# Kernel optimization log

Hardware: AMD Instinct MI355X
Metric: run time of the kernel (lower is better)

Reference implementation:

```python
import jax, jax.numpy as jnp
import numpy as np

B, P, D, H, A, C = 256, 512, 16, 256, 8, 2
HID = 256
IN_MLP = H + A + 1  # 265


def setup_inputs() -> dict:
    key = jax.random.key(0)
    ks = jax.random.split(key, 12)
    s = 0.05  # small init for recurrent stability
    return {
        "particles": jax.random.normal(ks[0], (B, P, D), jnp.float32),
        "weights": jax.random.uniform(ks[1], (B, P), jnp.float32),
        "actions": jax.random.normal(ks[2], (B, A), jnp.float32),
        "time": jax.random.uniform(ks[3], (B,), jnp.float32) * 100.0,
        "Wi": jax.random.normal(ks[4], (D + 1, 3 * H), jnp.float32) * s,
        "bi": jnp.zeros((3 * H,), jnp.float32),
        "Wh_rz": jax.random.normal(ks[5], (H, 2 * H), jnp.float32) * s,
        "Wh_n": jax.random.normal(ks[6], (H, H), jnp.float32) * s,
        "bn": jnp.zeros((H,), jnp.float32),
        "mlp_W1": jax.random.normal(ks[7], (C, IN_MLP, HID), jnp.float32) * s,
        "mlp_b1": jnp.zeros((C, HID), jnp.float32),
        "mlp_W2": jax.random.normal(ks[8], (C, HID, HID), jnp.float32) * s,
        "mlp_b2": jnp.zeros((C, HID), jnp.float32),
        "mlp_W3": jax.random.normal(ks[9], (C, HID, 1), jnp.float32) * s,
        "mlp_b3": jnp.zeros((C, 1), jnp.float32),
        "num_time_steps": 100,
    }


def reference(particles, weights, actions, time, Wi, bi, Wh_rz, Wh_n, bn,
              mlp_W1, mlp_b1, mlp_W2, mlp_b2, mlp_W3, mlp_b3, num_time_steps):
    # feature_fn = identity; append weights as an extra feature channel
    x = jnp.concatenate([particles, weights[..., None]], axis=-1)  # [B, P, D+1]
    xs = jnp.swapaxes(x, 0, 1)  # [P, B, D+1], scan over particle axis

    def gru_step(h, xt):
        gi = xt @ Wi + bi  # [B, 3H]
        i_r, i_z, i_n = jnp.split(gi, 3, axis=-1)
        hrz = h @ Wh_rz  # [B, 2H], no bias (flax GRUCell hidden r/z dense)
        r = jax.nn.sigmoid(i_r + hrz[:, :H])
        z = jax.nn.sigmoid(i_z + hrz[:, H:])
        n = jnp.tanh(i_n + r * (h @ Wh_n + bn))
        h_new = (1.0 - z) * n + z * h
        return h_new, None

    h0 = jnp.zeros((particles.shape[0], H), particles.dtype)
    enc, _ = jax.lax.scan(gru_step, h0, xs)  # last hidden == take(outputs, -1, axis=-2)

    norm_time = time / num_time_steps
    hidden = jnp.concatenate([enc, actions, norm_time[..., None]], axis=-1)  # [B, IN_MLP]

    # n_critics MLPs evaluated batched over critic axis c
    h1 = jax.nn.relu(jnp.einsum('bi,cio->bco', hidden, mlp_W1) + mlp_b1)
    h2 = jax.nn.relu(jnp.einsum('bci,cio->bco', h1, mlp_W2) + mlp_b2)
    q = jnp.einsum('bci,cio->bco', h2, mlp_W3) + mlp_b3  # [B, C, 1]
    return q[..., 0]  # [B, C]
```

## Files before the change

kernel.cpp:

```cpp
#include <hip/hip_runtime.h>
#include <hip/hip_fp16.h>

typedef _Float16 h2v __attribute__((ext_vector_type(2)));
typedef _Float16 f16x8 __attribute__((ext_vector_type(8)));
typedef float f32x4 __attribute__((ext_vector_type(4)));
typedef unsigned int u32;
typedef unsigned short u16;

#define NB 256
#define NP 512
#define NH 256

#define OFF_WH 0
#define LEN_WH 98304
#define OFF_WIB (OFF_WH + LEN_WH)
#define LEN_WIB 12288
#define OFF_W1 (OFF_WIB + LEN_WIB)
#define LEN_W1 68096
#define OFF_W2 (OFF_W1 + LEN_W1)
#define LEN_W2 65536
#define OFF_W3 (OFF_W2 + LEN_W2)
#define LEN_W3 256
#define WS_DWORDS (OFF_W3 + LEN_W3)

__device__ __forceinline__ u32 pack2(float lo, float hi) {
    h2v v; v.x = (_Float16)lo; v.y = (_Float16)hi;
    return __builtin_bit_cast(u32, v);
}

__device__ __forceinline__ float fdot2(u32 a, u32 b, float c) {
#if __has_builtin(__builtin_amdgcn_fdot2)
    return __builtin_amdgcn_fdot2(__builtin_bit_cast(h2v, a),
                                  __builtin_bit_cast(h2v, b), c, false);
#else
    h2v x = __builtin_bit_cast(h2v, a), y = __builtin_bit_cast(h2v, b);
    return c + (float)x.x * (float)y.x + (float)x.y * (float)y.y;
#endif
}

__global__ __launch_bounds__(256) void pack_kernel(
    const float* __restrict__ Wi, const float* __restrict__ Whrz,
    const float* __restrict__ Whn, const float* __restrict__ W1,
    const float* __restrict__ W2, const float* __restrict__ W3,
    u32* __restrict__ ws)
{
    for (int F = blockIdx.x * 256 + threadIdx.x; F < WS_DWORDS; F += gridDim.x * 256) {
        u32 val;
        if (F < OFF_WIB) {
            int d = F & 3; int r = F >> 2;
            int l = r & 63; int q = r >> 6;
            int f = q % 48; int w = q / 48;
            int t = f >> 3; int kt = f & 7;
            int g = t >> 1, c = t & 1;
            int k = kt * 32 + ((l >> 4) << 3) + 2 * d;
            int col = g * 256 + w * 32 + c * 16 + (l & 15);
            float lo, hi;
            if (col < 512) { lo = Whrz[k * 512 + col]; hi = Whrz[(k + 1) * 512 + col]; }
            else { lo = Whn[k * 256 + (col - 512)]; hi = Whn[(k + 1) * 256 + (col - 512)]; }
            val = pack2(lo, hi);
        } else if (F < OFF_W1) {
            int j = F - OFF_WIB;
            int d = j & 3; int r = j >> 2;
            int l = r & 63; int q2 = r >> 6;
            int t = q2 % 6; int w = q2 / 6;
            int g = t >> 1, c = t & 1;
            int k = ((l >> 4) << 3) + 2 * d;
            int col = g * 256 + w * 32 + c * 16 + (l & 15);
            float lo = (k < 17) ? Wi[k * 768 + col] : 0.f;
            float hi = (k + 1 < 17) ? Wi[(k + 1) * 768 + col] : 0.f;
            val = pack2(lo, hi);
        } else if (F < OFF_W2) {
            int j = F - OFF_W1; int c = j / (133 * 256); int r = j % (133 * 256);
            int kk = r >> 8; int o = r & 255;
            int k = 2 * kk;
            float lo = W1[(c * 265 + k) * 256 + o];
            float hi = (k + 1 < 265) ? W1[(c * 265 + k + 1) * 256 + o] : 0.f;
            val = pack2(lo, hi);
        } else if (F < OFF_W3) {
            int j = F - OFF_W2; int c = j >> 15; int r = j & 32767;
            int kk = r >> 8; int o = r & 255;
            float lo = W2[(c * 256 + 2 * kk) * 256 + o];
            float hi = W2[(c * 256 + 2 * kk + 1) * 256 + o];
            val = pack2(lo, hi);
        } else {
            int j = F - OFF_W3; int c = j >> 7; int jj = j & 127;
            float lo = W3[c * 256 + 2 * jj];
            float hi = W3[c * 256 + 2 * jj + 1];
            val = pack2(lo, hi);
        }
        ws[F] = val;
    }
}

#define MFMA_AB(acc, av, bf) \
    asm volatile("v_mfma_f32_16x16x32_f16 %0, %1, %2, %0" \
                 : "+v"(acc) : "v"(av), "a"(bf))

__global__ __launch_bounds__(512, 2) void qnet_kernel(
    const float* __restrict__ particles, const float* __restrict__ pweights,
    const float* __restrict__ actions, const float* __restrict__ timev,
    const float* __restrict__ bi, const float* __restrict__ bn,
    const float* __restrict__ b1, const float* __restrict__ b2,
    const float* __restrict__ b3, const int* __restrict__ nts,
    const u32* __restrict__ ws, float* __restrict__ out)
{
    __shared__ __align__(16) u32 sX[NP * 16];
    __shared__ __align__(16) float sG[8 * 1536];
    __shared__ __align__(16) u16 sH2[2][NH];
    __shared__ __align__(16) float sHf[NH];
    __shared__ __align__(16) float sMisc[16];

    const int b = blockIdx.x;
    const int tid = threadIdx.x;
    const int lane = tid & 63;
    const int wid = tid >> 6;

    f16x8 bfh[48];
    {
        const uint4* gp = (const uint4*)(ws + OFF_WH) + (wid * 48) * 64 + lane;
        #pragma unroll
        for (int i = 0; i < 48; ++i) bfh[i] = __builtin_bit_cast(f16x8, gp[i * 64]);
    }
    {
        const float2* pr2 = (const float2*)(particles + (long)b * NP * 16);
        for (int j = tid; j < NP * 8; j += 512) {
            int p = j >> 3, q = j & 7;
            float2 v = pr2[j];
            sX[p * 16 + q] = pack2(v.x, v.y);
        }
        const float* wr = pweights + (long)b * NP;
        for (int j = tid; j < NP * 8; j += 512) {
            int p = j >> 3, q = j & 7;
            sX[p * 16 + 8 + q] = (q == 0) ? pack2(wr[p], 0.f) : 0u;
        }
    }
    if (tid < 256) ((u32*)sH2)[tid] = 0u;
    if (tid < 8) sMisc[tid] = actions[b * 8 + tid];
    if (tid == 8) sMisc[8] = timev[b] / (float)nts[0];

    float birL = 0.f, bizL = 0.f, binnL = 0.f, bnnL = 0.f, hreg = 0.f;
    if (lane < 32) {
        int j = wid * 32 + lane;
        birL = bi[j]; bizL = bi[NH + j]; binnL = bi[2 * NH + j]; bnnL = bn[j];
    }
    __syncthreads();

    const uint4* wibp = (const uint4*)(ws + OFF_WIB) + (wid * 6) * 64 + lane;

    #pragma unroll 1
    for (int p = 0; p < NP; ++p) {
        if ((p & 15) == 0) {
            f16x8 av = __builtin_bit_cast(f16x8,
                ((const uint4*)sX)[(p + (lane & 15)) * 4 + (lane >> 4)]);
            f32x4 z4 = {0.f, 0.f, 0.f, 0.f};
            int sb = (lane >> 4) << 2;
            float* gw = sG + wid * 1536 + (lane & 15);
            {
                f32x4 g0 = __builtin_amdgcn_mfma_f32_16x16x32_f16(av, __builtin_bit_cast(f16x8, wibp[0 * 64]), z4, 0, 0, 0);
                f32x4 g1 = __builtin_amdgcn_mfma_f32_16x16x32_f16(av, __builtin_bit_cast(f16x8, wibp[1 * 64]), z4, 0, 0, 0);
                #pragma unroll
                for (int r = 0; r < 4; ++r) {
                    gw[(sb + r) * 32]      = g0[r];
                    gw[(sb + r) * 32 + 16] = g1[r];
                }
            }
            {
                f32x4 g2 = __builtin_amdgcn_mfma_f32_16x16x32_f16(av, __builtin_bit_cast(f16x8, wibp[2 * 64]), z4, 0, 0, 0);
                f32x4 g3 = __builtin_amdgcn_mfma_f32_16x16x32_f16(av, __builtin_bit_cast(f16x8, wibp[3 * 64]), z4, 0, 0, 0);
                #pragma unroll
                for (int r = 0; r < 4; ++r) {
                    gw[512 + (sb + r) * 32]      = g2[r];
                    gw[512 + (sb + r) * 32 + 16] = g3[r];
                }
            }
            {
                f32x4 g4 = __builtin_amdgcn_mfma_f32_16x16x32_f16(av, __builtin_bit_cast(f16x8, wibp[4 * 64]), z4, 0, 0, 0);
                f32x4 g5 = __builtin_amdgcn_mfma_f32_16x16x32_f16(av, __builtin_bit_cast(f16x8, wibp[5 * 64]), z4, 0, 0, 0);
                #pragma unroll
                for (int r = 0; r < 4; ++r) {
                    gw[1024 + (sb + r) * 32]      = g4[r];
                    gw[1024 + (sb + r) * 32 + 16] = g5[r];
                }
            }
            __syncthreads();
        }

        float gR, gZ, gN;
        {
            const float* gp = sG + wid * 1536 + (p & 15) * 32 + (lane & 31);
            gR = gp[0]; gZ = gp[512]; gN = gp[1024];
        }

        const u32* hbuf = (const u32*)(&sH2[p & 1][0]);
        f32x4 a0 = {0.f, 0.f, 0.f, 0.f}, a1 = a0, a2 = a0, a3 = a0, a4 = a0, a5 = a0;
        asm volatile("s_nop 1\n\ts_nop 1"
                     : "+v"(a0), "+v"(a1), "+v"(a2), "+v"(a3), "+v"(a4), "+v"(a5));
        #pragma unroll
        for (int kt = 0; kt < 8; ++kt) {
            f16x8 hv = __builtin_bit_cast(f16x8, ((const uint4*)hbuf)[kt * 4 + (lane >> 4)]);
            MFMA_AB(a0, hv, bfh[kt]);
            MFMA_AB(a1, hv, bfh[8 + kt]);
            MFMA_AB(a2, hv, bfh[16 + kt]);
            MFMA_AB(a3, hv, bfh[24 + kt]);
            MFMA_AB(a4, hv, bfh[32 + kt]);
            MFMA_AB(a5, hv, bfh[40 + kt]);
        }
        asm volatile("s_nop 7\n\ts_nop 7\n\ts_nop 7"
                     : "+v"(a0), "+v"(a1), "+v"(a2), "+v"(a3), "+v"(a4), "+v"(a5));

        bool hic = (lane & 16) != 0;
        float srm = hic ? a1[0] : a0[0];
        float szm = hic ? a3[0] : a2[0];
        float snm = hic ? a5[0] : a4[0];
        if (lane < 32) {
            float xr = gR + birL + srm;
            float xz = gZ + bizL + szm;
            float xn = gN + binnL;
            float r = 1.f / (1.f + __expf(-xr));
            float z = 1.f / (1.f + __expf(-xz));
            float targ = xn + r * (snm + bnnL);
            float e2 = __expf(2.f * targ);
            float n = 1.f - 2.f / (e2 + 1.f);
            hreg = (1.f - z) * n + z * hreg;
            _Float16 hh = (_Float16)hreg;
            sH2[(p + 1) & 1][wid * 32 + lane] = __builtin_bit_cast(u16, hh);
        }
        __syncthreads();
    }

    if (lane < 32) sHf[wid * 32 + lane] = hreg;
    __syncthreads();
    u32* sHid = (u32*)sG;
    u16* sL1 = (u16*)(sG + 512);
    u16* sL2 = (u16*)(sG + 1024);
    if (tid < 128) sHid[tid] = pack2(sHf[2 * tid], sHf[2 * tid + 1]);
    else if (tid < 132) { int i = tid - 128; sHid[tid] = pack2(sMisc[2 * i], sMisc[2 * i + 1]); }
    else if (tid == 132) sHid[132] = pack2(sMisc[8], 0.f);
    __syncthreads();
    {
        int c = tid >> 8, o = tid & 255;
        float acc = b1[c * 256 + o];
        const u32* wp = ws + OFF_W1 + c * 133 * 256 + o;
        #pragma unroll 4
        for (int kk = 0; kk < 133; ++kk) acc = fdot2(wp[kk * 256], sHid[kk], acc);
        acc = fmaxf(acc, 0.f);
        _Float16 a16 = (_Float16)acc;
        sL1[tid] = __builtin_bit_cast(u16, a16);
    }
    __syncthreads();
    {
        int c = tid >> 8, o = tid & 255;
        float acc = b2[c * 256 + o];
        const u32* wp = ws + OFF_W2 + c * 128 * 256 + o;
        const u32* hp = (const u32*)sL1 + c * 128;
        #pragma unroll 4
        for (int kk = 0; kk < 128; ++kk) acc = fdot2(wp[kk * 256], hp[kk], acc);
        acc = fmaxf(acc, 0.f);
        _Float16 a16 = (_Float16)acc;
        sL2[tid] = __builtin_bit_cast(u16, a16);
    }
    __syncthreads();
    if (tid < 128) {
        int c = tid >> 6, l = tid & 63;
        const u32* wp = ws + OFF_W3 + c * 128;
        const u32* hp = (const u32*)sL2 + c * 128;
        float acc = fdot2(wp[l], hp[l], 0.f);
        acc = fdot2(wp[64 + l], hp[64 + l], acc);
        #pragma unroll
        for (int off = 32; off > 0; off >>= 1) acc += __shfl_down(acc, off);
        if (l == 0) out[b * 2 + c] = acc + b3[c];
    }
}

extern "C" void kernel_launch(void* const* d_in, const int* in_sizes, int n_in,
                              void* d_out, int out_size, void* d_ws, size_t ws_size,
                              hipStream_t stream) {
    const float* particles = (const float*)d_in[0];
    const float* pweights  = (const float*)d_in[1];
    const float* actions   = (const float*)d_in[2];
    const float* timev     = (const float*)d_in[3];
    const float* Wi        = (const float*)d_in[4];
    const float* bi        = (const float*)d_in[5];
    const float* Whrz      = (const float*)d_in[6];
    const float* Whn       = (const float*)d_in[7];
    const float* bn        = (const float*)d_in[8];
    const float* W1        = (const float*)d_in[9];
    const float* b1        = (const float*)d_in[10];
    const float* W2        = (const float*)d_in[11];
    const float* b2        = (const float*)d_in[12];
    const float* W3        = (const float*)d_in[13];
    const float* b3        = (const float*)d_in[14];
    const int*   nts       = (const int*)d_in[15];
    u32* ws = (u32*)d_ws;
    float* outp = (float*)d_out;

    pack_kernel<<<(WS_DWORDS + 255) / 256, 256, 0, stream>>>(Wi, Whrz, Whn, W1, W2, W3, ws);
    qnet_kernel<<<NB, 512, 0, stream>>>(particles, pweights, actions, timev,
                                        bi, bn, b1, b2, b3, nts, ws, outp);
}
```

Before: 757.3 us.

## Stream recurrent weights from global/LDS instead of registers, stage particles per chunk

The kernel no longer keeps the 48 recurrent weight fragments in AGPRs. It reads the r/z weight fragments from global memory on every step and stages the n-gate weights in a 128KB LDS buffer. Particles are now prefetched 16 at a time into a small LDS buffer instead of staging all 512 up front. The input-gate projections are stored as fp16 to shrink LDS use. This cuts register pressure and inline-asm nops, but it adds global and LDS traffic on the serial critical path of every recurrence step, and the fp16 gate storage lowers precision.

```diff
diff --git a/kernel.cpp b/kernel.cpp
--- a/kernel.cpp
+++ b/kernel.cpp
@@ -92,10 +92,6 @@
     }
 }
 
-#define MFMA_AB(acc, av, bf) \
-    asm volatile("v_mfma_f32_16x16x32_f16 %0, %1, %2, %0" \
-                 : "+v"(acc) : "v"(av), "a"(bf))
-
 __global__ __launch_bounds__(512, 2) void qnet_kernel(
     const float* __restrict__ particles, const float* __restrict__ pweights,
     const float* __restrict__ actions, const float* __restrict__ timev,
@@ -104,8 +100,9 @@
     const float* __restrict__ b3, const int* __restrict__ nts,
     const u32* __restrict__ ws, float* __restrict__ out)
 {
-    __shared__ __align__(16) u32 sX[NP * 16];
-    __shared__ __align__(16) float sG[8 * 1536];
+    __shared__ __align__(16) u32 sWn[32768];
+    __shared__ __align__(16) u16 sGh[8 * 1536];
+    __shared__ __align__(16) u32 sXc[256];
     __shared__ __align__(16) u16 sH2[2][NH];
     __shared__ __align__(16) float sHf[NH];
     __shared__ __align__(16) float sMisc[16];
@@ -115,25 +112,9 @@
     const int lane = tid & 63;
     const int wid = tid >> 6;
 
-    f16x8 bfh[48];
-    {
-        const uint4* gp = (const uint4*)(ws + OFF_WH) + (wid * 48) * 64 + lane;
-        #pragma unroll
-        for (int i = 0; i < 48; ++i) bfh[i] = __builtin_bit_cast(f16x8, gp[i * 64]);
-    }
-    {
-        const float2* pr2 = (const float2*)(particles + (long)b * NP * 16);
-        for (int j = tid; j < NP * 8; j += 512) {
-            int p = j >> 3, q = j & 7;
-            float2 v = pr2[j];
-            sX[p * 16 + q] = pack2(v.x, v.y);
-        }
-        const float* wr = pweights + (long)b * NP;
-        for (int j = tid; j < NP * 8; j += 512) {
-            int p = j >> 3, q = j & 7;
-            sX[p * 16 + 8 + q] = (q == 0) ? pack2(wr[p], 0.f) : 0u;
-        }
-    }
+    for (int j = tid; j < 32768; j += 512)
+        sWn[j] = ws[OFF_WH + j + ((j >> 12) + 1) * 8192];
+
     if (tid < 256) ((u32*)sH2)[tid] = 0u;
     if (tid < 8) sMisc[tid] = actions[b * 8 + tid];
     if (tid == 8) sMisc[8] = timev[b] / (float)nts[0];
@@ -143,25 +124,45 @@
         int j = wid * 32 + lane;
         birL = bi[j]; bizL = bi[NH + j]; binnL = bi[2 * NH + j]; bnnL = bn[j];
     }
+
+    const int xs = tid >> 4;
+    const int xd = tid & 15;
+    float2 pv = {0.f, 0.f}; float wv = 0.f;
+    if (tid < 256) {
+        if (xd < 8) pv = *(const float2*)(particles + ((long)b * NP + xs) * 16 + 2 * xd);
+        else if (xd == 8) wv = pweights[(long)b * NP + xs];
+    }
     __syncthreads();
 
     const uint4* wibp = (const uint4*)(ws + OFF_WIB) + (wid * 6) * 64 + lane;
+    const uint4* gpr = (const uint4*)(ws + OFF_WH) + (wid * 48) * 64 + lane;
+    const uint4* wn  = ((const uint4*)sWn) + (wid * 16) * 64 + lane;
+    const int hq = lane >> 4;
 
     #pragma unroll 1
     for (int p = 0; p < NP; ++p) {
         if ((p & 15) == 0) {
+            if (tid < 256) {
+                u32 v;
+                if (xd < 8) v = pack2(pv.x, pv.y);
+                else if (xd == 8) v = pack2(wv, 0.f);
+                else v = 0u;
+                sXc[xs * 16 + xd] = v;
+            }
+            __syncthreads();
             f16x8 av = __builtin_bit_cast(f16x8,
-                ((const uint4*)sX)[(p + (lane & 15)) * 4 + (lane >> 4)]);
+                ((const uint4*)sXc)[(lane & 15) * 4 + (lane >> 4)]);
             f32x4 z4 = {0.f, 0.f, 0.f, 0.f};
             int sb = (lane >> 4) << 2;
-            float* gw = sG + wid * 1536 + (lane & 15);
+            int c16 = lane & 15;
+            u16* gw = sGh + wid * 1536;
             {
                 f32x4 g0 = __builtin_amdgcn_mfma_f32_16x16x32_f16(av, __builtin_bit_cast(f16x8, wibp[0 * 64]), z4, 0, 0, 0);
                 f32x4 g1 = __builtin_amdgcn_mfma_f32_16x16x32_f16(av, __builtin_bit_cast(f16x8, wibp[1 * 64]), z4, 0, 0, 0);
                 #pragma unroll
                 for (int r = 0; r < 4; ++r) {
-                    gw[(sb + r) * 32]      = g0[r];
-                    gw[(sb + r) * 32 + 16] = g1[r];
+                    gw[(sb + r) * 32 + c16]      = __builtin_bit_cast(u16, (_Float16)g0[r]);
+                    gw[(sb + r) * 32 + c16 + 16] = __builtin_bit_cast(u16, (_Float16)g1[r]);
                 }
             }
             {
@@ -169,8 +170,8 @@
                 f32x4 g3 = __builtin_amdgcn_mfma_f32_16x16x32_f16(av, __builtin_bit_cast(f16x8, wibp[3 * 64]), z4, 0, 0, 0);
                 #pragma unroll
                 for (int r = 0; r < 4; ++r) {
-                    gw[512 + (sb + r) * 32]      = g2[r];
-                    gw[512 + (sb + r) * 32 + 16] = g3[r];
+                    gw[512 + (sb + r) * 32 + c16]      = __builtin_bit_cast(u16, (_Float16)g2[r]);
+                    gw[512 + (sb + r) * 32 + c16 + 16] = __builtin_bit_cast(u16, (_Float16)g3[r]);
                 }
             }
             {
@@ -178,35 +179,38 @@
                 f32x4 g5 = __builtin_amdgcn_mfma_f32_16x16x32_f16(av, __builtin_bit_cast(f16x8, wibp[5 * 64]), z4, 0, 0, 0);
                 #pragma unroll
                 for (int r = 0; r < 4; ++r) {
-                    gw[1024 + (sb + r) * 32]      = g4[r];
-                    gw[1024 + (sb + r) * 32 + 16] = g5[r];
+                    gw[1024 + (sb + r) * 32 + c16]      = __builtin_bit_cast(u16, (_Float16)g4[r]);
+                    gw[1024 + (sb + r) * 32 + c16 + 16] = __builtin_bit_cast(u16, (_Float16)g5[r]);
                 }
+            }
+            if (tid < 256 && p + 16 < NP) {
+                int ps = p + 16 + xs;
+                if (xd < 8) pv = *(const float2*)(particles + ((long)b * NP + ps) * 16 + 2 * xd);
+                else if (xd == 8) wv = pweights[(long)b * NP + ps];
             }
             __syncthreads();
         }
 
         float gR, gZ, gN;
         {
-            const float* gp = sG + wid * 1536 + (p & 15) * 32 + (lane & 31);
-            gR = gp[0]; gZ = gp[512]; gN = gp[1024];
+            const u16* gp = sGh + wid * 1536 + (p & 15) * 32 + (lane & 31);
+            gR = (float)__builtin_bit_cast(_Float16, gp[0]);
+            gZ = (float)__builtin_bit_cast(_Float16, gp[512]);
+            gN = (float)__builtin_bit_cast(_Float16, gp[1024]);
         }
 
         const u32* hbuf = (const u32*)(&sH2[p & 1][0]);
         f32x4 a0 = {0.f, 0.f, 0.f, 0.f}, a1 = a0, a2 = a0, a3 = a0, a4 = a0, a5 = a0;
-        asm volatile("s_nop 1\n\ts_nop 1"
-                     : "+v"(a0), "+v"(a1), "+v"(a2), "+v"(a3), "+v"(a4), "+v"(a5));
         #pragma unroll
         for (int kt = 0; kt < 8; ++kt) {
-            f16x8 hv = __builtin_bit_cast(f16x8, ((const uint4*)hbuf)[kt * 4 + (lane >> 4)]);
-            MFMA_AB(a0, hv, bfh[kt]);
-            MFMA_AB(a1, hv, bfh[8 + kt]);
-            MFMA_AB(a2, hv, bfh[16 + kt]);
-            MFMA_AB(a3, hv, bfh[24 + kt]);
-            MFMA_AB(a4, hv, bfh[32 + kt]);
-            MFMA_AB(a5, hv, bfh[40 + kt]);
-        }
-        asm volatile("s_nop 7\n\ts_nop 7\n\ts_nop 7"
-                     : "+v"(a0), "+v"(a1), "+v"(a2), "+v"(a3), "+v"(a4), "+v"(a5));
+            f16x8 hv = __builtin_bit_cast(f16x8, ((const uint4*)hbuf)[kt * 4 + hq]);
+            a0 = __builtin_amdgcn_mfma_f32_16x16x32_f16(hv, __builtin_bit_cast(f16x8, gpr[kt * 64]),        a0, 0, 0, 0);
+            a1 = __builtin_amdgcn_mfma_f32_16x16x32_f16(hv, __builtin_bit_cast(f16x8, gpr[(8 + kt) * 64]),  a1, 0, 0, 0);
+            a2 = __builtin_amdgcn_mfma_f32_16x16x32_f16(hv, __builtin_bit_cast(f16x8, gpr[(16 + kt) * 64]), a2, 0, 0, 0);
+            a3 = __builtin_amdgcn_mfma_f32_16x16x32_f16(hv, __builtin_bit_cast(f16x8, gpr[(24 + kt) * 64]), a3, 0, 0, 0);
+            a4 = __builtin_amdgcn_mfma_f32_16x16x32_f16(hv, __builtin_bit_cast(f16x8, wn[kt * 64]),         a4, 0, 0, 0);
+            a5 = __builtin_amdgcn_mfma_f32_16x16x32_f16(hv, __builtin_bit_cast(f16x8, wn[(8 + kt) * 64]),   a5, 0, 0, 0);
+        }
 
         bool hic = (lane & 16) != 0;
         float srm = hic ? a1[0] : a0[0];
@@ -230,9 +234,9 @@
 
     if (lane < 32) sHf[wid * 32 + lane] = hreg;
     __syncthreads();
-    u32* sHid = (u32*)sG;
-    u16* sL1 = (u16*)(sG + 512);
-    u16* sL2 = (u16*)(sG + 1024);
+    u32* sHid = sWn;
+    u16* sL1 = (u16*)(sWn + 256);
+    u16* sL2 = (u16*)(sWn + 640);
     if (tid < 128) sHid[tid] = pack2(sHf[2 * tid], sHf[2 * tid + 1]);
     else if (tid < 132) { int i = tid - 128; sHid[tid] = pack2(sMisc[2 * i], sMisc[2 * i + 1]); }
     else if (tid == 132) sHid[132] = pack2(sMisc[8], 0.f);
```

Result: faster. 666.2 us (-12.0%).
